# Kernel tuning notes

Measured on AMD Instinct MI355X. Metric: run time of the kernel, lower is better.

The kernel has to match this reference:

```python
import jax, jax.numpy as jnp
import numpy as np

DIM = 256
HEADS = 8
DK = DIM // HEADS
MLP_HID = 4 * DIM
EPS = 1e-5


def _ln(t, s, b):
    m = jnp.mean(t, axis=-1, keepdims=True)
    v = jnp.mean((t - m) ** 2, axis=-1, keepdims=True)
    return (t - m) / jnp.sqrt(v + EPS) * s + b


def setup_inputs() -> dict:
    key = jax.random.key(0)
    ks = jax.random.split(key, 32)
    B, N, C = 8, 128, DIM
    d = {}
    d["x"] = jax.random.normal(ks[0], (B, N, C), jnp.float32)
    d["y"] = jax.random.normal(ks[1], (B, N, N, C), jnp.float32)
    def lin(k, fi, fo):
        k1, k2 = jax.random.split(k)
        return (jax.random.normal(k1, (fi, fo), jnp.float32) * 0.02,
                jax.random.normal(k2, (fo,), jnp.float32) * 0.02)
    for i, nm in enumerate(["q", "k", "v", "e", "oe", "on"]):
        w, b = lin(ks[2 + i], C, C)
        d[f"W{nm}"], d[f"b{nm}"] = w, b
    for i, nm in enumerate(["mlp1", "mlp2"]):
        w1, b1 = lin(ks[10 + 2 * i], C, MLP_HID)
        w2, b2 = lin(ks[11 + 2 * i], MLP_HID, C)
        d[f"{nm}_w1"], d[f"{nm}_b1"] = w1, b1
        d[f"{nm}_w2"], d[f"{nm}_b2"] = w2, b2
    for i, nm in enumerate(["ln1", "ln3", "ln4", "ln5", "ln6"]):
        d[f"{nm}_s"] = jnp.ones((C,), jnp.float32)
        d[f"{nm}_b"] = jnp.zeros((C,), jnp.float32)
    return d


def reference(x, y, Wq, bq, Wk, bk, Wv, bv, We, be, Woe, boe, Won, bon,
              mlp1_w1, mlp1_b1, mlp1_w2, mlp1_b2,
              mlp2_w1, mlp2_b1, mlp2_w2, mlp2_b2,
              ln1_s, ln1_b, ln3_s, ln3_b, ln4_s, ln4_b,
              ln5_s, ln5_b, ln6_s, ln6_b):
    B, N, C = x.shape
    H, DKl = HEADS, DK

    x1 = _ln(x, ln1_s, ln1_b)

    # attention (elementwise q*k modulated by edge embeddings)
    q = (x1 @ Wq + bq).reshape(B, N, H, DKl)
    k = (x1 @ Wk + bk).reshape(B, N, H, DKl)
    v = (x1 @ Wv + bv).reshape(B, N, H, DKl)
    e = (y @ We + be).reshape(B, N, N, H, DKl)

    attn = q[:, :, None] * k[:, None, :]          # (B,N,N,H,DK)
    attn = attn / jnp.sqrt(jnp.float32(DKl))
    attn = attn * (e + 1.0) * e

    edge_out = attn.reshape(B, N, N, C) @ Woe + boe  # out_e
    p = jax.nn.softmax(attn, axis=2)                 # softmax over second n
    agg = jnp.einsum("bijhd,bjhd->bihd", p, v).reshape(B, N, C)
    node_out = agg @ Won + bon                       # out_n

    x2 = _ln(x1 + node_out, ln3_s, ln3_b)
    y2 = _ln(edge_out + y, ln4_s, ln4_b)

    mlp_x = jax.nn.relu(x2 @ mlp1_w1 + mlp1_b1) @ mlp1_w2 + mlp1_b2
    mlp_y = jax.nn.relu(y2 @ mlp2_w1 + mlp2_b1) @ mlp2_w2 + mlp2_b2

    x_out = _ln(x2 + mlp_x, ln5_s, ln5_b)
    y_out = _ln(y2 + mlp_y, ln6_s, ln6_b)
    return (x_out, y_out)
```

## Files before the change

kernel.cpp:

```cpp
#include <hip/hip_runtime.h>

#define CDIM 256
#define NSEQ 128
#define HID 1024
#define EPS 1e-5f
#define SCALE 0.17677669529663687f
#define ASTR 264
#define MROWS 32

typedef __attribute__((ext_vector_type(8))) short short8;
typedef __attribute__((ext_vector_type(4))) float f32x4;

static __device__ __forceinline__ unsigned short f2bf(float x) {
    unsigned u = __float_as_uint(x);
    u += 0x7fff + ((u >> 16) & 1);
    return (unsigned short)(u >> 16);
}
static __device__ __forceinline__ float bf2f(unsigned short h) {
    return __uint_as_float(((unsigned)h) << 16);
}

__global__ __launch_bounds__(256) void prep_all(
    const float* __restrict__ We, const float* __restrict__ Woe,
    const float* __restrict__ W1, const float* __restrict__ W2,
    unsigned short* __restrict__ WeH, unsigned short* __restrict__ WeL,
    unsigned short* __restrict__ WoH, unsigned short* __restrict__ W1H,
    unsigned short* __restrict__ W2H) {
    int blk = blockIdx.x;
    const float* W; unsigned short* H; unsigned short* L = nullptr;
    int N, ksBits, base;
    if (blk < 256)       { W = We;  H = WeH; L = WeL; N = 256;  ksBits = 3; base = 0; }
    else if (blk < 512)  { W = Woe; H = WoH; N = 256;  ksBits = 3; base = 256; }
    else if (blk < 1536) { W = W1;  H = W1H; N = 1024; ksBits = 3; base = 512; }
    else                 { W = W2;  H = W2H; N = 256;  ksBits = 5; base = 1536; }
    int idx = (blk - base) * 256 + threadIdx.x;
    int j = idx & 7, lane = (idx >> 3) & 63, rest = idx >> 9;
    int ks = rest & ((1 << ksBits) - 1), nt = rest >> ksBits;
    int n  = nt * 16 + (lane & 15);
    int kk = ks * 32 + ((lane >> 4) << 3) + j;
    float x = W[kk * N + n];
    unsigned short h = f2bf(x);
    H[idx] = h;
    if (L) L[idx] = f2bf(x - bf2f(h));
}

__global__ __launch_bounds__(256) void lnqkv_kernel(
    const float* __restrict__ x,
    const float* __restrict__ ln1s, const float* __restrict__ ln1b,
    const float* __restrict__ Wq, const float* __restrict__ bq,
    const float* __restrict__ Wk, const float* __restrict__ bk,
    const float* __restrict__ Wv, const float* __restrict__ bv,
    float* __restrict__ x1,
    float* __restrict__ q, float* __restrict__ k, float* __restrict__ v) {
    __shared__ float sX[4][CDIM];
    __shared__ float sMu[4], sRs[4];
    const int bi0 = blockIdx.x * 4, t = threadIdx.x;
    const int w = t >> 6, lane = t & 63;
    float xv[4];
    #pragma unroll
    for (int r = 0; r < 4; ++r) { xv[r] = x[(bi0 + r) * CDIM + t]; sX[r][t] = xv[r]; }
    __syncthreads();
    {
        float s = 0.f, ss = 0.f;
        #pragma unroll
        for (int m = 0; m < 4; ++m) { float a = sX[w][lane + 64 * m]; s += a; ss += a * a; }
        #pragma unroll
        for (int off = 32; off; off >>= 1) { s += __shfl_xor(s, off); ss += __shfl_xor(ss, off); }
        if (lane == 0) {
            float mu = s * (1.f / 256.f);
            sMu[w] = mu;
            sRs[w] = rsqrtf(ss * (1.f / 256.f) - mu * mu + EPS);
        }
    }
    __syncthreads();
    #pragma unroll
    for (int r = 0; r < 4; ++r) {
        float xn = (xv[r] - sMu[r]) * sRs[r] * ln1s[t] + ln1b[t];
        sX[r][t] = xn;
        x1[(bi0 + r) * CDIM + t] = xn;
    }
    __syncthreads();
    float aq[4], ak[4], av[4];
    #pragma unroll
    for (int r = 0; r < 4; ++r) { aq[r] = bq[t]; ak[r] = bk[t]; av[r] = bv[t]; }
    #pragma unroll 4
    for (int kk = 0; kk < CDIM; ++kk) {
        float wq = Wq[kk * CDIM + t], wk = Wk[kk * CDIM + t], wv = Wv[kk * CDIM + t];
        #pragma unroll
        for (int r = 0; r < 4; ++r) {
            float xd = sX[r][kk];
            aq[r] += xd * wq; ak[r] += xd * wk; av[r] += xd * wv;
        }
    }
    #pragma unroll
    for (int r = 0; r < 4; ++r) {
        q[(bi0 + r) * CDIM + t] = aq[r];
        k[(bi0 + r) * CDIM + t] = ak[r];
        v[(bi0 + r) * CDIM + t] = av[r];
    }
}

template <int TERMS>
static __device__ __forceinline__ void gemmN(
    const unsigned short* Ah, const unsigned short* Al,
    const unsigned short* __restrict__ Bh, const unsigned short* __restrict__ Bl,
    int nt0, int ksTotal, int ks0, int lane, f32x4 acc[2][2])
{
    const int l16 = lane & 15, quad = lane >> 4;
    #pragma unroll 2
    for (int ks = 0; ks < 8; ++ks) {
        short8 bh[2], bl[2];
        #pragma unroll
        for (int nt = 0; nt < 2; ++nt) {
            size_t off = ((size_t)((nt0 + nt) * ksTotal + (ks0 + ks)) * 64 + lane) * 8;
            bh[nt] = *(const short8*)(Bh + off);
            if (TERMS == 3) bl[nt] = *(const short8*)(Bl + off);
        }
        #pragma unroll
        for (int mt = 0; mt < 2; ++mt) {
            int ao = (mt * 16 + l16) * ASTR + ks * 32 + quad * 8;
            short8 ah = *(const short8*)(Ah + ao);
            short8 al = *(const short8*)(Al + ao);
            #pragma unroll
            for (int nt = 0; nt < 2; ++nt) {
                acc[mt][nt] = __builtin_amdgcn_mfma_f32_16x16x32_bf16(ah, bh[nt], acc[mt][nt], 0, 0, 0);
                acc[mt][nt] = __builtin_amdgcn_mfma_f32_16x16x32_bf16(al, bh[nt], acc[mt][nt], 0, 0, 0);
                if (TERMS == 3)
                    acc[mt][nt] = __builtin_amdgcn_mfma_f32_16x16x32_bf16(ah, bl[nt], acc[mt][nt], 0, 0, 0);
            }
        }
    }
}

static __device__ __forceinline__ void ln_reduce32(
    float pre[2][2][4], float* sSum, float* sSS, int w, int l16, int quad, int tid)
{
    #pragma unroll
    for (int mt = 0; mt < 2; ++mt)
        #pragma unroll
        for (int r = 0; r < 4; ++r) {
            float s  = pre[mt][0][r] + pre[mt][1][r];
            float ss = pre[mt][0][r] * pre[mt][0][r] + pre[mt][1][r] * pre[mt][1][r];
            #pragma unroll
            for (int off = 1; off < 16; off <<= 1) {
                s  += __shfl_xor(s, off);
                ss += __shfl_xor(ss, off);
            }
            if (l16 == 0) {
                int row = mt * 16 + quad * 4 + r;
                sSum[w * 32 + row] = s;
                sSS [w * 32 + row] = ss;
            }
        }
    __syncthreads();
    if (tid < 32) {
        float S = 0.f, SS2 = 0.f;
        #pragma unroll
        for (int ww = 0; ww < 8; ++ww) { S += sSum[ww * 32 + tid]; SS2 += sSS[ww * 32 + tid]; }
        float mu = S * (1.f / 256.f);
        float rs = rsqrtf(SS2 * (1.f / 256.f) - mu * mu + EPS);
        sSum[tid] = mu; sSS[tid] = rs;
    }
    __syncthreads();
}

__global__ __launch_bounds__(512, 4) void y_mega(
    const float* __restrict__ y, const float* __restrict__ qg, const float* __restrict__ kg,
    const unsigned short* __restrict__ WeH, const unsigned short* __restrict__ WeL,
    const float* __restrict__ be,
    const unsigned short* __restrict__ WoH, const float* __restrict__ boe,
    const unsigned short* __restrict__ W1H, const float* __restrict__ b1,
    const unsigned short* __restrict__ W2H, const float* __restrict__ b2,
    const float* __restrict__ ln4s, const float* __restrict__ ln4b,
    const float* __restrict__ ln6s, const float* __restrict__ ln6b,
    unsigned short* __restrict__ attn_bf, float* __restrict__ yout)
{
    __shared__ unsigned short sAh[MROWS * ASTR], sAl[MROWS * ASTR];
    __shared__ unsigned short sHh[MROWS * ASTR], sHl[MROWS * ASTR];
    __shared__ float sSum[8 * 32], sSS[8 * 32];

    const int tid  = threadIdx.x;
    const int w    = tid >> 6, lane = tid & 63;
    const int l16  = lane & 15, quad = lane >> 4;
    const long long row0 = (long long)blockIdx.x * MROWS;
    const int b  = (int)(row0 >> 14);
    const int i  = (int)((row0 >> 7) & 127);
    const int j0 = (int)(row0 & 127);
    const float* qrow  = qg + ((b << 7) + i) * CDIM;
    const float* kbase = kg + ((b << 7) + j0) * CDIM;
    const int c0 = w * 32 + l16, c1 = c0 + 16;

    {
        int r  = tid >> 4;
        int cc = (tid & 15) * 16;
        const float* src = y + (row0 + r) * CDIM + cc;
        unsigned short hbuf[16], lbuf[16];
        #pragma unroll
        for (int e = 0; e < 16; e += 4) {
            float4 vv = *(const float4*)(src + e);
            float a[4] = {vv.x, vv.y, vv.z, vv.w};
            #pragma unroll
            for (int d = 0; d < 4; ++d) {
                unsigned short h = f2bf(a[d]);
                hbuf[e + d] = h;
                lbuf[e + d] = f2bf(a[d] - bf2f(h));
            }
        }
        #pragma unroll
        for (int e = 0; e < 16; e += 8) {
            *(short8*)&sAh[r * ASTR + cc + e] = *(short8*)&hbuf[e];
            *(short8*)&sAl[r * ASTR + cc + e] = *(short8*)&lbuf[e];
        }
    }
    __syncthreads();

    f32x4 acc[2][2];
    const f32x4 zf = {0.f, 0.f, 0.f, 0.f};

    #pragma unroll
    for (int mt = 0; mt < 2; ++mt) { acc[mt][0] = zf; acc[mt][1] = zf; }
    gemmN<3>(sAh, sAl, WeH, WeL, w * 2, 8, 0, lane, acc);

    float q0 = qrow[c0], q1 = qrow[c1];
    float be0 = be[c0], be1 = be[c1];
    float attnv[2][2][4];
    #pragma unroll
    for (int mt = 0; mt < 2; ++mt)
        #pragma unroll
        for (int r = 0; r < 4; ++r) {
            int mloc = mt * 16 + quad * 4 + r;
            float k0 = kbase[mloc * CDIM + c0], k1 = kbase[mloc * CDIM + c1];
            float e0 = acc[mt][0][r] + be0, e1 = acc[mt][1][r] + be1;
            float a0 = q0 * k0 * SCALE * ((e0 + 1.f) * e0);
            float a1 = q1 * k1 * SCALE * ((e1 + 1.f) * e1);
            attnv[mt][0][r] = a0; attnv[mt][1][r] = a1;
            attn_bf[(row0 + mloc) * CDIM + c0] = f2bf(a0);
            attn_bf[(row0 + mloc) * CDIM + c1] = f2bf(a1);
        }
    __syncthreads();

    #pragma unroll
    for (int mt = 0; mt < 2; ++mt)
        #pragma unroll
        for (int r = 0; r < 4; ++r) {
            int mloc = mt * 16 + quad * 4 + r;
            #pragma unroll
            for (int nt = 0; nt < 2; ++nt) {
                int c = (nt == 0) ? c0 : c1;
                float a = attnv[mt][nt][r];
                unsigned short h = f2bf(a);
                sAh[mloc * ASTR + c] = h;
                sAl[mloc * ASTR + c] = f2bf(a - bf2f(h));
            }
        }
    __syncthreads();

    #pragma unroll
    for (int mt = 0; mt < 2; ++mt) { acc[mt][0] = zf; acc[mt][1] = zf; }
    gemmN<2>(sAh, sAl, WoH, nullptr, w * 2, 8, 0, lane, acc);

    float pre[2][2][4];
    float bo0 = boe[c0], bo1 = boe[c1];
    #pragma unroll
    for (int mt = 0; mt < 2; ++mt)
        #pragma unroll
        for (int r = 0; r < 4; ++r) {
            int mloc = mt * 16 + quad * 4 + r;
            pre[mt][0][r] = acc[mt][0][r] + bo0 + y[(row0 + mloc) * CDIM + c0];
            pre[mt][1][r] = acc[mt][1][r] + bo1 + y[(row0 + mloc) * CDIM + c1];
        }
    ln_reduce32(pre, sSum, sSS, w, l16, quad, tid);

    float l4s0 = ln4s[c0], l4b0 = ln4b[c0], l4s1 = ln4s[c1], l4b1 = ln4b[c1];
    float y2v[2][2][4];
    #pragma unroll
    for (int mt = 0; mt < 2; ++mt)
        #pragma unroll
        for (int r = 0; r < 4; ++r) {
            int mloc = mt * 16 + quad * 4 + r;
            float mu = sSum[mloc], rs = sSS[mloc];
            float v0 = (pre[mt][0][r] - mu) * rs * l4s0 + l4b0;
            float v1 = (pre[mt][1][r] - mu) * rs * l4s1 + l4b1;
            y2v[mt][0][r] = v0; y2v[mt][1][r] = v1;
            unsigned short h0 = f2bf(v0), h1 = f2bf(v1);
            sAh[mloc * ASTR + c0] = h0; sAl[mloc * ASTR + c0] = f2bf(v0 - bf2f(h0));
            sAh[mloc * ASTR + c1] = h1; sAl[mloc * ASTR + c1] = f2bf(v1 - bf2f(h1));
        }
    __syncthreads();

    f32x4 out[2][2];
    #pragma unroll
    for (int mt = 0; mt < 2; ++mt) { out[mt][0] = zf; out[mt][1] = zf; }
    for (int qq = 0; qq < 4; ++qq) {
        f32x4 hh[2][2];
        #pragma unroll
        for (int mt = 0; mt < 2; ++mt) { hh[mt][0] = zf; hh[mt][1] = zf; }
        gemmN<2>(sAh, sAl, W1H, nullptr, qq * 16 + w * 2, 8, 0, lane, hh);
        float bb0 = b1[qq * 256 + c0], bb1 = b1[qq * 256 + c1];
        __syncthreads();
        #pragma unroll
        for (int mt = 0; mt < 2; ++mt)
            #pragma unroll
            for (int r = 0; r < 4; ++r) {
                int mloc = mt * 16 + quad * 4 + r;
                float h0 = fmaxf(hh[mt][0][r] + bb0, 0.f);
                float h1 = fmaxf(hh[mt][1][r] + bb1, 0.f);
                unsigned short hb0 = f2bf(h0), hb1 = f2bf(h1);
                sHh[mloc * ASTR + c0] = hb0; sHl[mloc * ASTR + c0] = f2bf(h0 - bf2f(hb0));
                sHh[mloc * ASTR + c1] = hb1; sHl[mloc * ASTR + c1] = f2bf(h1 - bf2f(hb1));
            }
        __syncthreads();
        gemmN<2>(sHh, sHl, W2H, nullptr, w * 2, 32, qq * 8, lane, out);
    }

    float b20 = b2[c0], b21 = b2[c1];
    #pragma unroll
    for (int mt = 0; mt < 2; ++mt)
        #pragma unroll
        for (int r = 0; r < 4; ++r) {
            pre[mt][0][r] = y2v[mt][0][r] + out[mt][0][r] + b20;
            pre[mt][1][r] = y2v[mt][1][r] + out[mt][1][r] + b21;
        }
    ln_reduce32(pre, sSum, sSS, w, l16, quad, tid);

    float l6s0 = ln6s[c0], l6b0 = ln6b[c0], l6s1 = ln6s[c1], l6b1 = ln6b[c1];
    #pragma unroll
    for (int mt = 0; mt < 2; ++mt)
        #pragma unroll
        for (int r = 0; r < 4; ++r) {
            int mloc = mt * 16 + quad * 4 + r;
            float mu = sSum[mloc], rs = sSS[mloc];
            yout[(row0 + mloc) * CDIM + c0] = (pre[mt][0][r] - mu) * rs * l6s0 + l6b0;
            yout[(row0 + mloc) * CDIM + c1] = (pre[mt][1][r] - mu) * rs * l6s1 + l6b1;
        }
}

__global__ __launch_bounds__(256) void softmax_agg(
    const unsigned short* __restrict__ attn, const float* __restrict__ v,
    float* __restrict__ agg) {
    __shared__ float2 sM[2][128], sS[2][128], sO[2][128];
    const int bi = blockIdx.x, t = threadIdx.x;
    const int c2 = t & 127, team = t >> 7, ch = c2 * 2;
    const unsigned short* ap = attn + (size_t)bi * NSEQ * CDIM + ch;
    const float* vp = v + (size_t)(bi >> 7) * NSEQ * CDIM + ch;
    const int jb = team * 64;
    float m0 = -1e30f, m1 = -1e30f;
    #pragma unroll 4
    for (int j = jb; j < jb + 64; ++j) {
        unsigned uu = *(const unsigned*)(ap + (size_t)j * CDIM);
        m0 = fmaxf(m0, bf2f((unsigned short)uu));
        m1 = fmaxf(m1, bf2f((unsigned short)(uu >> 16)));
    }
    sM[team][c2] = make_float2(m0, m1);
    __syncthreads();
    float2 mo = sM[team ^ 1][c2];
    m0 = fmaxf(m0, mo.x); m1 = fmaxf(m1, mo.y);
    float s0 = 0.f, s1 = 0.f, o0 = 0.f, o1 = 0.f;
    #pragma unroll 4
    for (int j = jb; j < jb + 64; ++j) {
        unsigned uu = *(const unsigned*)(ap + (size_t)j * CDIM);
        float e0 = __expf(bf2f((unsigned short)uu) - m0);
        float e1 = __expf(bf2f((unsigned short)(uu >> 16)) - m1);
        float2 vv = *(const float2*)(vp + (size_t)j * CDIM);
        s0 += e0; s1 += e1;
        o0 += e0 * vv.x; o1 += e1 * vv.y;
    }
    sS[team][c2] = make_float2(s0, s1);
    sO[team][c2] = make_float2(o0, o1);
    __syncthreads();
    if (team == 0) {
        float2 s2 = sS[1][c2], o2 = sO[1][c2];
        float r0 = (o0 + o2.x) / (s0 + s2.x);
        float r1 = (o1 + o2.y) / (s1 + s2.y);
        *(float2*)(agg + (size_t)bi * CDIM + ch) = make_float2(r0, r1);
    }
}

__global__ __launch_bounds__(256) void x_path(
    const float* __restrict__ x1, const float* __restrict__ agg,
    const float* __restrict__ Won, const float* __restrict__ bon,
    const float* __restrict__ ln3s, const float* __restrict__ ln3b,
    const float* __restrict__ w1, const float* __restrict__ b1,
    const float* __restrict__ w2, const float* __restrict__ b2,
    const float* __restrict__ ln5s, const float* __restrict__ ln5b,
    float* __restrict__ xout) {
    __shared__ float sG[4][CDIM];
    __shared__ float sP[4][CDIM];
    __shared__ float sH[4][HID];
    __shared__ float sMu[4], sRs[4];
    const int bi0 = blockIdx.x * 4, t = threadIdx.x;
    const int w = t >> 6, lane = t & 63;
    #pragma unroll
    for (int r = 0; r < 4; ++r) sG[r][t] = agg[(bi0 + r) * CDIM + t];
    __syncthreads();
    float no[4];
    #pragma unroll
    for (int r = 0; r < 4; ++r) no[r] = bon[t];
    #pragma unroll 4
    for (int kk = 0; kk < CDIM; ++kk) {
        float wv = Won[kk * CDIM + t];
        #pragma unroll
        for (int r = 0; r < 4; ++r) no[r] += sG[r][kk] * wv;
    }
    float pre[4];
    #pragma unroll
    for (int r = 0; r < 4; ++r) {
        pre[r] = x1[(bi0 + r) * CDIM + t] + no[r];
        sP[r][t] = pre[r];
    }
    __syncthreads();
    {
        float s = 0.f, ss = 0.f;
        #pragma unroll
        for (int m = 0; m < 4; ++m) { float a = sP[w][lane + 64 * m]; s += a; ss += a * a; }
        #pragma unroll
        for (int off = 32; off; off >>= 1) { s += __shfl_xor(s, off); ss += __shfl_xor(ss, off); }
        if (lane == 0) {
            float mu = s * (1.f / 256.f);
            sMu[w] = mu; sRs[w] = rsqrtf(ss * (1.f / 256.f) - mu * mu + EPS);
        }
    }
    __syncthreads();
    float x2[4];
    #pragma unroll
    for (int r = 0; r < 4; ++r) {
        x2[r] = (pre[r] - sMu[r]) * sRs[r] * ln3s[t] + ln3b[t];
        sP[r][t] = x2[r];
    }
    __syncthreads();
    float h[4][4];
    #pragma unroll
    for (int m = 0; m < 4; ++m) {
        float bb = b1[t + 256 * m];
        #pragma unroll
        for (int r = 0; r < 4; ++r) h[r][m] = bb;
    }
    #pragma unroll 2
    for (int kk = 0; kk < CDIM; ++kk) {
        float wv[4];
        #pragma unroll
        for (int m = 0; m < 4; ++m) wv[m] = w1[kk * HID + t + 256 * m];
        #pragma unroll
        for (int r = 0; r < 4; ++r) {
            float xd = sP[r][kk];
            #pragma unroll
            for (int m = 0; m < 4; ++m) h[r][m] += xd * wv[m];
        }
    }
    #pragma unroll
    for (int r = 0; r < 4; ++r)
        #pragma unroll
        for (int m = 0; m < 4; ++m) sH[r][t + 256 * m] = fmaxf(h[r][m], 0.f);
    __syncthreads();
    float o[4];
    #pragma unroll
    for (int r = 0; r < 4; ++r) o[r] = b2[t];
    #pragma unroll 4
    for (int u = 0; u < HID; ++u) {
        float wv = w2[u * CDIM + t];
        #pragma unroll
        for (int r = 0; r < 4; ++r) o[r] += sH[r][u] * wv;
    }
    float pre2[4];
    #pragma unroll
    for (int r = 0; r < 4; ++r) { pre2[r] = x2[r] + o[r]; sP[r][t] = pre2[r]; }
    __syncthreads();
    {
        float s = 0.f, ss = 0.f;
        #pragma unroll
        for (int m = 0; m < 4; ++m) { float a = sP[w][lane + 64 * m]; s += a; ss += a * a; }
        #pragma unroll
        for (int off = 32; off; off >>= 1) { s += __shfl_xor(s, off); ss += __shfl_xor(ss, off); }
        if (lane == 0) {
            float mu = s * (1.f / 256.f);
            sMu[w] = mu; sRs[w] = rsqrtf(ss * (1.f / 256.f) - mu * mu + EPS);
        }
    }
    __syncthreads();
    #pragma unroll
    for (int r = 0; r < 4; ++r)
        xout[(bi0 + r) * CDIM + t] = (pre2[r] - sMu[r]) * sRs[r] * ln5s[t] + ln5b[t];
}

extern "C" void kernel_launch(void* const* d_in, const int* in_sizes, int n_in,
                              void* d_out, int out_size, void* d_ws, size_t ws_size,
                              hipStream_t stream) {
    const float* x   = (const float*)d_in[0];
    const float* y   = (const float*)d_in[1];
    const float* Wq  = (const float*)d_in[2];  const float* bq  = (const float*)d_in[3];
    const float* Wk  = (const float*)d_in[4];  const float* bk  = (const float*)d_in[5];
    const float* Wv  = (const float*)d_in[6];  const float* bv  = (const float*)d_in[7];
    const float* We  = (const float*)d_in[8];  const float* be  = (const float*)d_in[9];
    const float* Woe = (const float*)d_in[10]; const float* boe = (const float*)d_in[11];
    const float* Won = (const float*)d_in[12]; const float* bon = (const float*)d_in[13];
    const float* m1w1= (const float*)d_in[14]; const float* m1b1= (const float*)d_in[15];
    const float* m1w2= (const float*)d_in[16]; const float* m1b2= (const float*)d_in[17];
    const float* m2w1= (const float*)d_in[18]; const float* m2b1= (const float*)d_in[19];
    const float* m2w2= (const float*)d_in[20]; const float* m2b2= (const float*)d_in[21];
    const float* ln1s= (const float*)d_in[22]; const float* ln1b= (const float*)d_in[23];
    const float* ln3s= (const float*)d_in[24]; const float* ln3b= (const float*)d_in[25];
    const float* ln4s= (const float*)d_in[26]; const float* ln4b= (const float*)d_in[27];
    const float* ln5s= (const float*)d_in[28]; const float* ln5b= (const float*)d_in[29];
    const float* ln6s= (const float*)d_in[30]; const float* ln6b= (const float*)d_in[31];

    const int BN  = 8 * 128;
    const long long BNN = 8LL * 128 * 128;

    float* ws  = (float*)d_ws;
    float* x1  = ws;
    float* q   = x1 + BN * CDIM;
    float* k   = q  + BN * CDIM;
    float* v   = k  + BN * CDIM;
    float* agg = v  + BN * CDIM;
    unsigned short* attn_bf = (unsigned short*)(agg + BN * CDIM);
    unsigned short* WeH = attn_bf + BNN * CDIM;
    unsigned short* WeL = WeH + 65536;
    unsigned short* WoH = WeL + 65536;
    unsigned short* W1H = WoH + 65536;
    unsigned short* W2H = W1H + 262144;

    float* xout = (float*)d_out;
    float* yout = xout + BN * CDIM;

    prep_all<<<2560, 256, 0, stream>>>(We, Woe, m2w1, m2w2, WeH, WeL, WoH, W1H, W2H);
    lnqkv_kernel<<<BN / 4, 256, 0, stream>>>(x, ln1s, ln1b, Wq, bq, Wk, bk, Wv, bv,
                                             x1, q, k, v);
    y_mega<<<(int)(BNN / MROWS), 512, 0, stream>>>(
        y, q, k, WeH, WeL, be, WoH, boe, W1H, m2b1, W2H, m2b2,
        ln4s, ln4b, ln6s, ln6b, attn_bf, yout);
    softmax_agg<<<BN, 256, 0, stream>>>(attn_bf, v, agg);
    x_path<<<BN / 4, 256, 0, stream>>>(x1, agg, Won, bon, ln3s, ln3b,
                                       m1w1, m1b1, m1w2, m1b2, ln5s, ln5b, xout);
}
```

Before: 880.3 us.

## Restructure y_mega to 4 waves with 64-column tiles and XOR-swizzled LDS

The fused edge kernel goes from 8 waves owning 32 columns each to 4 waves owning 64 columns each, so every A-fragment read from LDS feeds twice as many MFMAs. Padded LDS rows are replaced by an XOR swizzle, and the MLP hidden chunk shrinks to 128 columns, which cuts shared memory. bf16 hi/lo splits now use the packed v_cvt_pk_bf16_f32 instruction. In exchange each thread holds more accumulators, which raises register pressure, and fewer waves per block may hide latency less well.

```diff
diff --git a/kernel.cpp b/kernel.cpp
--- a/kernel.cpp
+++ b/kernel.cpp
@@ -5,7 +5,6 @@
 #define HID 1024
 #define EPS 1e-5f
 #define SCALE 0.17677669529663687f
-#define ASTR 264
 #define MROWS 32
 
 typedef __attribute__((ext_vector_type(8))) short short8;
@@ -19,6 +18,14 @@
 static __device__ __forceinline__ float bf2f(unsigned short h) {
     return __uint_as_float(((unsigned)h) << 16);
 }
+
+static __device__ __forceinline__ unsigned cvt_pk(float a, float b) {
+    unsigned r;
+    asm("v_cvt_pk_bf16_f32 %0, %1, %2" : "=v"(r) : "v"(a), "v"(b));
+    return r;
+}
+
+static __device__ __forceinline__ int swz(int row) { return (row ^ (row >> 2)) & 7; }
 
 __global__ __launch_bounds__(256) void prep_all(
     const float* __restrict__ We, const float* __restrict__ Woe,
@@ -100,29 +107,30 @@
     }
 }
 
-template <int TERMS>
+template <int TERMS, int NT, int KS, int LDA>
 static __device__ __forceinline__ void gemmN(
     const unsigned short* Ah, const unsigned short* Al,
     const unsigned short* __restrict__ Bh, const unsigned short* __restrict__ Bl,
-    int nt0, int ksTotal, int ks0, int lane, f32x4 acc[2][2])
+    int nt0, int ksTotal, int ks0, int lane, f32x4 acc[2][NT])
 {
     const int l16 = lane & 15, quad = lane >> 4;
     #pragma unroll 2
-    for (int ks = 0; ks < 8; ++ks) {
-        short8 bh[2], bl[2];
-        #pragma unroll
-        for (int nt = 0; nt < 2; ++nt) {
+    for (int ks = 0; ks < KS; ++ks) {
+        short8 bh[NT], bl[NT];
+        #pragma unroll
+        for (int nt = 0; nt < NT; ++nt) {
             size_t off = ((size_t)((nt0 + nt) * ksTotal + (ks0 + ks)) * 64 + lane) * 8;
             bh[nt] = *(const short8*)(Bh + off);
             if (TERMS == 3) bl[nt] = *(const short8*)(Bl + off);
         }
         #pragma unroll
         for (int mt = 0; mt < 2; ++mt) {
-            int ao = (mt * 16 + l16) * ASTR + ks * 32 + quad * 8;
+            const int row = mt * 16 + l16;
+            const int ao  = row * LDA + (((ks * 4 + quad) ^ swz(row)) << 3);
             short8 ah = *(const short8*)(Ah + ao);
             short8 al = *(const short8*)(Al + ao);
             #pragma unroll
-            for (int nt = 0; nt < 2; ++nt) {
+            for (int nt = 0; nt < NT; ++nt) {
                 acc[mt][nt] = __builtin_amdgcn_mfma_f32_16x16x32_bf16(ah, bh[nt], acc[mt][nt], 0, 0, 0);
                 acc[mt][nt] = __builtin_amdgcn_mfma_f32_16x16x32_bf16(al, bh[nt], acc[mt][nt], 0, 0, 0);
                 if (TERMS == 3)
@@ -132,15 +140,19 @@
     }
 }
 
-static __device__ __forceinline__ void ln_reduce32(
-    float pre[2][2][4], float* sSum, float* sSS, int w, int l16, int quad, int tid)
+static __device__ __forceinline__ void ln_reduce32_4w(
+    float pre[2][4][4], float* sSum, float* sSS, int w, int l16, int quad, int tid)
 {
     #pragma unroll
     for (int mt = 0; mt < 2; ++mt)
         #pragma unroll
         for (int r = 0; r < 4; ++r) {
-            float s  = pre[mt][0][r] + pre[mt][1][r];
-            float ss = pre[mt][0][r] * pre[mt][0][r] + pre[mt][1][r] * pre[mt][1][r];
+            float s = 0.f, ss = 0.f;
+            #pragma unroll
+            for (int nt = 0; nt < 4; ++nt) {
+                float a = pre[mt][nt][r];
+                s += a; ss += a * a;
+            }
             #pragma unroll
             for (int off = 1; off < 16; off <<= 1) {
                 s  += __shfl_xor(s, off);
@@ -156,7 +168,7 @@
     if (tid < 32) {
         float S = 0.f, SS2 = 0.f;
         #pragma unroll
-        for (int ww = 0; ww < 8; ++ww) { S += sSum[ww * 32 + tid]; SS2 += sSS[ww * 32 + tid]; }
+        for (int ww = 0; ww < 4; ++ww) { S += sSum[ww * 32 + tid]; SS2 += sSS[ww * 32 + tid]; }
         float mu = S * (1.f / 256.f);
         float rs = rsqrtf(SS2 * (1.f / 256.f) - mu * mu + EPS);
         sSum[tid] = mu; sSS[tid] = rs;
@@ -164,7 +176,7 @@
     __syncthreads();
 }
 
-__global__ __launch_bounds__(512, 4) void y_mega(
+__global__ __launch_bounds__(256, 3) void y_mega(
     const float* __restrict__ y, const float* __restrict__ qg, const float* __restrict__ kg,
     const unsigned short* __restrict__ WeH, const unsigned short* __restrict__ WeL,
     const float* __restrict__ be,
@@ -175,9 +187,9 @@
     const float* __restrict__ ln6s, const float* __restrict__ ln6b,
     unsigned short* __restrict__ attn_bf, float* __restrict__ yout)
 {
-    __shared__ unsigned short sAh[MROWS * ASTR], sAl[MROWS * ASTR];
-    __shared__ unsigned short sHh[MROWS * ASTR], sHl[MROWS * ASTR];
-    __shared__ float sSum[8 * 32], sSS[8 * 32];
+    __shared__ __align__(16) unsigned short sAh[32 * 256], sAl[32 * 256];
+    __shared__ __align__(16) unsigned short sHh[32 * 128], sHl[32 * 128];
+    __shared__ float sSum[4 * 32], sSS[4 * 32];
 
     const int tid  = threadIdx.x;
     const int w    = tid >> 6, lane = tid & 63;
@@ -188,150 +200,196 @@
     const int j0 = (int)(row0 & 127);
     const float* qrow  = qg + ((b << 7) + i) * CDIM;
     const float* kbase = kg + ((b << 7) + j0) * CDIM;
-    const int c0 = w * 32 + l16, c1 = c0 + 16;
+    int c[4];
+    #pragma unroll
+    for (int nt = 0; nt < 4; ++nt) c[nt] = w * 64 + nt * 16 + l16;
 
     {
-        int r  = tid >> 4;
-        int cc = (tid & 15) * 16;
-        const float* src = y + (row0 + r) * CDIM + cc;
-        unsigned short hbuf[16], lbuf[16];
-        #pragma unroll
-        for (int e = 0; e < 16; e += 4) {
-            float4 vv = *(const float4*)(src + e);
-            float a[4] = {vv.x, vv.y, vv.z, vv.w};
-            #pragma unroll
-            for (int d = 0; d < 4; ++d) {
-                unsigned short h = f2bf(a[d]);
-                hbuf[e + d] = h;
-                lbuf[e + d] = f2bf(a[d] - bf2f(h));
-            }
-        }
-        #pragma unroll
-        for (int e = 0; e < 16; e += 8) {
-            *(short8*)&sAh[r * ASTR + cc + e] = *(short8*)&hbuf[e];
-            *(short8*)&sAl[r * ASTR + cc + e] = *(short8*)&lbuf[e];
-        }
-    }
-    __syncthreads();
-
-    f32x4 acc[2][2];
+        const int r  = tid >> 3;
+        const int cb = (tid & 7) * 32;
+        const int fr = swz(r);
+        const float* src = y + (row0 + r) * CDIM + cb;
+        #pragma unroll
+        for (int gi = 0; gi < 4; ++gi) {
+            float4 v0 = *(const float4*)(src + gi * 8);
+            float4 v1 = *(const float4*)(src + gi * 8 + 4);
+            float a[8] = {v0.x, v0.y, v0.z, v0.w, v1.x, v1.y, v1.z, v1.w};
+            unsigned hw[4], lw[4];
+            #pragma unroll
+            for (int p = 0; p < 4; ++p) {
+                unsigned ph = cvt_pk(a[2 * p], a[2 * p + 1]);
+                float r0 = a[2 * p]     - __uint_as_float(ph << 16);
+                float r1 = a[2 * p + 1] - __uint_as_float(ph & 0xffff0000u);
+                hw[p] = ph;
+                lw[p] = cvt_pk(r0, r1);
+            }
+            const int gs = ((cb >> 3) + gi) ^ fr;
+            *(uint4*)&sAh[r * 256 + gs * 8] = *(const uint4*)hw;
+            *(uint4*)&sAl[r * 256 + gs * 8] = *(const uint4*)lw;
+        }
+    }
+    __syncthreads();
+
     const f32x4 zf = {0.f, 0.f, 0.f, 0.f};
-
-    #pragma unroll
-    for (int mt = 0; mt < 2; ++mt) { acc[mt][0] = zf; acc[mt][1] = zf; }
-    gemmN<3>(sAh, sAl, WeH, WeL, w * 2, 8, 0, lane, acc);
-
-    float q0 = qrow[c0], q1 = qrow[c1];
-    float be0 = be[c0], be1 = be[c1];
-    float attnv[2][2][4];
-    #pragma unroll
-    for (int mt = 0; mt < 2; ++mt)
-        #pragma unroll
-        for (int r = 0; r < 4; ++r) {
-            int mloc = mt * 16 + quad * 4 + r;
-            float k0 = kbase[mloc * CDIM + c0], k1 = kbase[mloc * CDIM + c1];
-            float e0 = acc[mt][0][r] + be0, e1 = acc[mt][1][r] + be1;
-            float a0 = q0 * k0 * SCALE * ((e0 + 1.f) * e0);
-            float a1 = q1 * k1 * SCALE * ((e1 + 1.f) * e1);
-            attnv[mt][0][r] = a0; attnv[mt][1][r] = a1;
-            attn_bf[(row0 + mloc) * CDIM + c0] = f2bf(a0);
-            attn_bf[(row0 + mloc) * CDIM + c1] = f2bf(a1);
-        }
-    __syncthreads();
-
-    #pragma unroll
-    for (int mt = 0; mt < 2; ++mt)
-        #pragma unroll
-        for (int r = 0; r < 4; ++r) {
-            int mloc = mt * 16 + quad * 4 + r;
-            #pragma unroll
-            for (int nt = 0; nt < 2; ++nt) {
-                int c = (nt == 0) ? c0 : c1;
-                float a = attnv[mt][nt][r];
-                unsigned short h = f2bf(a);
-                sAh[mloc * ASTR + c] = h;
-                sAl[mloc * ASTR + c] = f2bf(a - bf2f(h));
-            }
-        }
-    __syncthreads();
-
-    #pragma unroll
-    for (int mt = 0; mt < 2; ++mt) { acc[mt][0] = zf; acc[mt][1] = zf; }
-    gemmN<2>(sAh, sAl, WoH, nullptr, w * 2, 8, 0, lane, acc);
-
-    float pre[2][2][4];
-    float bo0 = boe[c0], bo1 = boe[c1];
-    #pragma unroll
-    for (int mt = 0; mt < 2; ++mt)
-        #pragma unroll
-        for (int r = 0; r < 4; ++r) {
-            int mloc = mt * 16 + quad * 4 + r;
-            pre[mt][0][r] = acc[mt][0][r] + bo0 + y[(row0 + mloc) * CDIM + c0];
-            pre[mt][1][r] = acc[mt][1][r] + bo1 + y[(row0 + mloc) * CDIM + c1];
-        }
-    ln_reduce32(pre, sSum, sSS, w, l16, quad, tid);
-
-    float l4s0 = ln4s[c0], l4b0 = ln4b[c0], l4s1 = ln4s[c1], l4b1 = ln4b[c1];
-    float y2v[2][2][4];
-    #pragma unroll
-    for (int mt = 0; mt < 2; ++mt)
-        #pragma unroll
-        for (int r = 0; r < 4; ++r) {
-            int mloc = mt * 16 + quad * 4 + r;
-            float mu = sSum[mloc], rs = sSS[mloc];
-            float v0 = (pre[mt][0][r] - mu) * rs * l4s0 + l4b0;
-            float v1 = (pre[mt][1][r] - mu) * rs * l4s1 + l4b1;
-            y2v[mt][0][r] = v0; y2v[mt][1][r] = v1;
-            unsigned short h0 = f2bf(v0), h1 = f2bf(v1);
-            sAh[mloc * ASTR + c0] = h0; sAl[mloc * ASTR + c0] = f2bf(v0 - bf2f(h0));
-            sAh[mloc * ASTR + c1] = h1; sAl[mloc * ASTR + c1] = f2bf(v1 - bf2f(h1));
-        }
-    __syncthreads();
-
-    f32x4 out[2][2];
-    #pragma unroll
-    for (int mt = 0; mt < 2; ++mt) { out[mt][0] = zf; out[mt][1] = zf; }
-    for (int qq = 0; qq < 4; ++qq) {
+    f32x4 acc[2][4];
+
+    #pragma unroll
+    for (int mt = 0; mt < 2; ++mt)
+        #pragma unroll
+        for (int nt = 0; nt < 4; ++nt) acc[mt][nt] = zf;
+    gemmN<3, 4, 8, 256>(sAh, sAl, WeH, WeL, w * 4, 8, 0, lane, acc);
+
+    float qv[4], bev[4];
+    #pragma unroll
+    for (int nt = 0; nt < 4; ++nt) { qv[nt] = qrow[c[nt]]; bev[nt] = be[c[nt]]; }
+    float attnv[2][4][4];
+    #pragma unroll
+    for (int mt = 0; mt < 2; ++mt)
+        #pragma unroll
+        for (int r = 0; r < 4; ++r) {
+            const int mloc = mt * 16 + quad * 4 + r;
+            const float* krow = kbase + mloc * CDIM;
+            #pragma unroll
+            for (int nt = 0; nt < 4; ++nt) {
+                float e = acc[mt][nt][r] + bev[nt];
+                attnv[mt][nt][r] = qv[nt] * krow[c[nt]] * SCALE * ((e + 1.f) * e);
+            }
+        }
+    __syncthreads();
+
+    #pragma unroll
+    for (int mt = 0; mt < 2; ++mt)
+        #pragma unroll
+        for (int r = 0; r < 4; ++r) {
+            const int mloc = mt * 16 + quad * 4 + r;
+            const int fr2  = swz(mloc);
+            unsigned short* gout = attn_bf + (row0 + mloc) * CDIM;
+            #pragma unroll
+            for (int np = 0; np < 4; np += 2) {
+                float a0 = attnv[mt][np][r], a1 = attnv[mt][np + 1][r];
+                unsigned ph = cvt_pk(a0, a1);
+                float r0 = a0 - __uint_as_float(ph << 16);
+                float r1 = a1 - __uint_as_float(ph & 0xffff0000u);
+                unsigned pl = cvt_pk(r0, r1);
+                const int aA = mloc * 256 + (((c[np]     >> 3) ^ fr2) << 3) + (l16 & 7);
+                const int aB = mloc * 256 + (((c[np + 1] >> 3) ^ fr2) << 3) + (l16 & 7);
+                sAh[aA] = (unsigned short)ph;  sAh[aB] = (unsigned short)(ph >> 16);
+                sAl[aA] = (unsigned short)pl;  sAl[aB] = (unsigned short)(pl >> 16);
+                gout[c[np]]     = (unsigned short)ph;
+                gout[c[np + 1]] = (unsigned short)(ph >> 16);
+            }
+        }
+    __syncthreads();
+
+    #pragma unroll
+    for (int mt = 0; mt < 2; ++mt)
+        #pragma unroll
+        for (int nt = 0; nt < 4; ++nt) acc[mt][nt] = zf;
+    gemmN<2, 4, 8, 256>(sAh, sAl, WoH, nullptr, w * 4, 8, 0, lane, acc);
+
+    float pre[2][4][4];
+    float bov[4];
+    #pragma unroll
+    for (int nt = 0; nt < 4; ++nt) bov[nt] = boe[c[nt]];
+    #pragma unroll
+    for (int mt = 0; mt < 2; ++mt)
+        #pragma unroll
+        for (int r = 0; r < 4; ++r) {
+            const int mloc = mt * 16 + quad * 4 + r;
+            const float* yrow = y + (row0 + mloc) * CDIM;
+            #pragma unroll
+            for (int nt = 0; nt < 4; ++nt)
+                pre[mt][nt][r] = acc[mt][nt][r] + bov[nt] + yrow[c[nt]];
+        }
+    ln_reduce32_4w(pre, sSum, sSS, w, l16, quad, tid);
+
+    float l4sv[4], l4bv[4];
+    #pragma unroll
+    for (int nt = 0; nt < 4; ++nt) { l4sv[nt] = ln4s[c[nt]]; l4bv[nt] = ln4b[c[nt]]; }
+    float y2v[2][4][4];
+    #pragma unroll
+    for (int mt = 0; mt < 2; ++mt)
+        #pragma unroll
+        for (int r = 0; r < 4; ++r) {
+            const int mloc = mt * 16 + quad * 4 + r;
+            const int fr2  = swz(mloc);
+            const float mu = sSum[mloc], rs = sSS[mloc];
+            #pragma unroll
+            for (int np = 0; np < 4; np += 2) {
+                float v0 = (pre[mt][np][r]     - mu) * rs * l4sv[np]     + l4bv[np];
+                float v1 = (pre[mt][np + 1][r] - mu) * rs * l4sv[np + 1] + l4bv[np + 1];
+                y2v[mt][np][r] = v0; y2v[mt][np + 1][r] = v1;
+                unsigned ph = cvt_pk(v0, v1);
+                float r0 = v0 - __uint_as_float(ph << 16);
+                float r1 = v1 - __uint_as_float(ph & 0xffff0000u);
+                unsigned pl = cvt_pk(r0, r1);
+                const int aA = mloc * 256 + (((c[np]     >> 3) ^ fr2) << 3) + (l16 & 7);
+                const int aB = mloc * 256 + (((c[np + 1] >> 3) ^ fr2) << 3) + (l16 & 7);
+                sAh[aA] = (unsigned short)ph;  sAh[aB] = (unsigned short)(ph >> 16);
+                sAl[aA] = (unsigned short)pl;  sAl[aB] = (unsigned short)(pl >> 16);
+            }
+        }
+    __syncthreads();
+
+    f32x4 out[2][4];
+    #pragma unroll
+    for (int mt = 0; mt < 2; ++mt)
+        #pragma unroll
+        for (int nt = 0; nt < 4; ++nt) out[mt][nt] = zf;
+    const int hc0 = w * 32 + l16, hc1 = hc0 + 16;
+    for (int ch = 0; ch < 8; ++ch) {
         f32x4 hh[2][2];
         #pragma unroll
         for (int mt = 0; mt < 2; ++mt) { hh[mt][0] = zf; hh[mt][1] = zf; }
-        gemmN<2>(sAh, sAl, W1H, nullptr, qq * 16 + w * 2, 8, 0, lane, hh);
-        float bb0 = b1[qq * 256 + c0], bb1 = b1[qq * 256 + c1];
+        gemmN<2, 2, 8, 256>(sAh, sAl, W1H, nullptr, ch * 8 + w * 2, 8, 0, lane, hh);
+        float bb0 = b1[ch * 128 + hc0], bb1 = b1[ch * 128 + hc1];
         __syncthreads();
         #pragma unroll
         for (int mt = 0; mt < 2; ++mt)
             #pragma unroll
             for (int r = 0; r < 4; ++r) {
-                int mloc = mt * 16 + quad * 4 + r;
+                const int mloc = mt * 16 + quad * 4 + r;
+                const int fr2  = swz(mloc);
                 float h0 = fmaxf(hh[mt][0][r] + bb0, 0.f);
                 float h1 = fmaxf(hh[mt][1][r] + bb1, 0.f);
-                unsigned short hb0 = f2bf(h0), hb1 = f2bf(h1);
-                sHh[mloc * ASTR + c0] = hb0; sHl[mloc * ASTR + c0] = f2bf(h0 - bf2f(hb0));
-                sHh[mloc * ASTR + c1] = hb1; sHl[mloc * ASTR + c1] = f2bf(h1 - bf2f(hb1));
+                unsigned ph = cvt_pk(h0, h1);
+                float r0 = h0 - __uint_as_float(ph << 16);
+                float r1 = h1 - __uint_as_float(ph & 0xffff0000u);
+                unsigned pl = cvt_pk(r0, r1);
+                const int aA = mloc * 128 + (((hc0 >> 3) ^ fr2) << 3) + (hc0 & 7);
+                const int aB = mloc * 128 + (((hc1 >> 3) ^ fr2) << 3) + (hc1 & 7);
+                sHh[aA] = (unsigned short)ph;  sHh[aB] = (unsigned short)(ph >> 16);
+                sHl[aA] = (unsigned short)pl;  sHl[aB] = (unsigned short)(pl >> 16);
             }
         __syncthreads();
-        gemmN<2>(sHh, sHl, W2H, nullptr, w * 2, 32, qq * 8, lane, out);
-    }
-
-    float b20 = b2[c0], b21 = b2[c1];
-    #pragma unroll
-    for (int mt = 0; mt < 2; ++mt)
-        #pragma unroll
-        for (int r = 0; r < 4; ++r) {
-            pre[mt][0][r] = y2v[mt][0][r] + out[mt][0][r] + b20;
-            pre[mt][1][r] = y2v[mt][1][r] + out[mt][1][r] + b21;
-        }
-    ln_reduce32(pre, sSum, sSS, w, l16, quad, tid);
-
-    float l6s0 = ln6s[c0], l6b0 = ln6b[c0], l6s1 = ln6s[c1], l6b1 = ln6b[c1];
-    #pragma unroll
-    for (int mt = 0; mt < 2; ++mt)
-        #pragma unroll
-        for (int r = 0; r < 4; ++r) {
-            int mloc = mt * 16 + quad * 4 + r;
-            float mu = sSum[mloc], rs = sSS[mloc];
-            yout[(row0 + mloc) * CDIM + c0] = (pre[mt][0][r] - mu) * rs * l6s0 + l6b0;
-            yout[(row0 + mloc) * CDIM + c1] = (pre[mt][1][r] - mu) * rs * l6s1 + l6b1;
+        gemmN<2, 4, 4, 128>(sHh, sHl, W2H, nullptr, w * 4, 32, ch * 4, lane, out);
+    }
+
+    float b2v[4];
+    #pragma unroll
+    for (int nt = 0; nt < 4; ++nt) b2v[nt] = b2[c[nt]];
+    #pragma unroll
+    for (int mt = 0; mt < 2; ++mt)
+        #pragma unroll
+        for (int r = 0; r < 4; ++r)
+            #pragma unroll
+            for (int nt = 0; nt < 4; ++nt)
+                pre[mt][nt][r] = y2v[mt][nt][r] + out[mt][nt][r] + b2v[nt];
+    ln_reduce32_4w(pre, sSum, sSS, w, l16, quad, tid);
+
+    float l6sv[4], l6bv[4];
+    #pragma unroll
+    for (int nt = 0; nt < 4; ++nt) { l6sv[nt] = ln6s[c[nt]]; l6bv[nt] = ln6b[c[nt]]; }
+    #pragma unroll
+    for (int mt = 0; mt < 2; ++mt)
+        #pragma unroll
+        for (int r = 0; r < 4; ++r) {
+            const int mloc = mt * 16 + quad * 4 + r;
+            const float mu = sSum[mloc], rs = sSS[mloc];
+            float* orow = yout + (row0 + mloc) * CDIM;
+            #pragma unroll
+            for (int nt = 0; nt < 4; ++nt)
+                orow[c[nt]] = (pre[mt][nt][r] - mu) * rs * l6sv[nt] + l6bv[nt];
         }
 }
 
@@ -525,7 +583,7 @@
     prep_all<<<2560, 256, 0, stream>>>(We, Woe, m2w1, m2w2, WeH, WeL, WoH, W1H, W2H);
     lnqkv_kernel<<<BN / 4, 256, 0, stream>>>(x, ln1s, ln1b, Wq, bq, Wk, bk, Wv, bv,
                                              x1, q, k, v);
-    y_mega<<<(int)(BNN / MROWS), 512, 0, stream>>>(
+    y_mega<<<(int)(BNN / MROWS), 256, 0, stream>>>(
         y, q, k, WeH, WeL, be, WoH, boe, W1H, m2b1, W2H, m2b2,
         ln4s, ln4b, ln6s, ln6b, attn_bf, yout);
     softmax_agg<<<BN, 256, 0, stream>>>(attn_bf, v, agg);
```

After: 971.0 us. 1.1x slower.

## Swizzle LDS operand tiles and pack bf16 hi/lo splits with paired lanes

Applied to the files above, without the earlier changes.

Replaces the padded shared-memory stride with an unpadded 256-wide layout and an XOR swizzle on 8-element groups. This is meant to avoid bank conflicts on the MFMA A-operand reads. The bf16 hi/lo split now uses the packed v_cvt_pk_bf16_f32 instruction, and neighbouring lanes exchange values by shuffle. Even lanes write the packed high plane and odd lanes the packed low plane, each as one 32-bit store, which cuts the number of conversions and scalar 16-bit stores. The cost is more shuffle traffic and an inline asm dependency on this instruction being available on the target.

```diff
diff --git a/kernel.cpp b/kernel.cpp
--- a/kernel.cpp
+++ b/kernel.cpp
@@ -5,7 +5,6 @@
 #define HID 1024
 #define EPS 1e-5f
 #define SCALE 0.17677669529663687f
-#define ASTR 264
 #define MROWS 32
 
 typedef __attribute__((ext_vector_type(8))) short short8;
@@ -19,6 +18,15 @@
 static __device__ __forceinline__ float bf2f(unsigned short h) {
     return __uint_as_float(((unsigned)h) << 16);
 }
+static __device__ __forceinline__ unsigned cvt_pk(float a, float b) {
+    unsigned r;
+    asm("v_cvt_pk_bf16_f32 %0, %1, %2" : "=v"(r) : "v"(a), "v"(b));
+    return r;
+}
+static __device__ __forceinline__ float lo16f(unsigned u) { return __uint_as_float(u << 16); }
+static __device__ __forceinline__ float hi16f(unsigned u) { return __uint_as_float(u & 0xffff0000u); }
+
+static __device__ __forceinline__ int swz(int row) { return (row ^ (row >> 2)) & 7; }
 
 __global__ __launch_bounds__(256) void prep_all(
     const float* __restrict__ We, const float* __restrict__ Woe,
@@ -118,7 +126,8 @@
         }
         #pragma unroll
         for (int mt = 0; mt < 2; ++mt) {
-            int ao = (mt * 16 + l16) * ASTR + ks * 32 + quad * 8;
+            const int row = mt * 16 + l16;
+            const int ao  = row * 256 + (((ks * 4 + quad) ^ swz(row)) << 3);
             short8 ah = *(const short8*)(Ah + ao);
             short8 al = *(const short8*)(Al + ao);
             #pragma unroll
@@ -164,6 +173,27 @@
     __syncthreads();
 }
 
+static __device__ __forceinline__ unsigned pair_pack(float v, bool odd, unsigned* ph_out) {
+    float part = __shfl_xor(v, 1);
+    float lo = odd ? part : v;
+    float hi = odd ? v : part;
+    unsigned ph = cvt_pk(lo, hi);
+    *ph_out = ph;
+    if (odd) {
+        float rlo = lo - lo16f(ph);
+        float rhi = hi - hi16f(ph);
+        return cvt_pk(rlo, rhi);
+    }
+    return ph;
+}
+static __device__ __forceinline__ void plane_store(
+    unsigned short* Hp, unsigned short* Lp, int row, int c, unsigned pk, bool odd) {
+    const int p = c & ~1;
+    const int idx = row * 256 + ((((p >> 3) ^ swz(row)) << 3)) + (p & 7);
+    if (!odd) *(unsigned*)&Hp[idx] = pk;
+    else      *(unsigned*)&Lp[idx] = pk;
+}
+
 __global__ __launch_bounds__(512, 4) void y_mega(
     const float* __restrict__ y, const float* __restrict__ qg, const float* __restrict__ kg,
     const unsigned short* __restrict__ WeH, const unsigned short* __restrict__ WeL,
@@ -175,13 +205,14 @@
     const float* __restrict__ ln6s, const float* __restrict__ ln6b,
     unsigned short* __restrict__ attn_bf, float* __restrict__ yout)
 {
-    __shared__ unsigned short sAh[MROWS * ASTR], sAl[MROWS * ASTR];
-    __shared__ unsigned short sHh[MROWS * ASTR], sHl[MROWS * ASTR];
+    __shared__ __align__(16) unsigned short sAh[32 * 256], sAl[32 * 256];
+    __shared__ __align__(16) unsigned short sHh[32 * 256], sHl[32 * 256];
     __shared__ float sSum[8 * 32], sSS[8 * 32];
 
     const int tid  = threadIdx.x;
     const int w    = tid >> 6, lane = tid & 63;
     const int l16  = lane & 15, quad = lane >> 4;
+    const bool odd = (l16 & 1) != 0;
     const long long row0 = (long long)blockIdx.x * MROWS;
     const int b  = (int)(row0 >> 14);
     const int i  = (int)((row0 >> 7) & 127);
@@ -191,25 +222,27 @@
     const int c0 = w * 32 + l16, c1 = c0 + 16;
 
     {
-        int r  = tid >> 4;
-        int cc = (tid & 15) * 16;
+        const int r  = tid >> 4;
+        const int cc = (tid & 15) * 16;
+        const int fr = swz(r);
         const float* src = y + (row0 + r) * CDIM + cc;
-        unsigned short hbuf[16], lbuf[16];
-        #pragma unroll
-        for (int e = 0; e < 16; e += 4) {
-            float4 vv = *(const float4*)(src + e);
-            float a[4] = {vv.x, vv.y, vv.z, vv.w};
-            #pragma unroll
-            for (int d = 0; d < 4; ++d) {
-                unsigned short h = f2bf(a[d]);
-                hbuf[e + d] = h;
-                lbuf[e + d] = f2bf(a[d] - bf2f(h));
-            }
-        }
         #pragma unroll
         for (int e = 0; e < 16; e += 8) {
-            *(short8*)&sAh[r * ASTR + cc + e] = *(short8*)&hbuf[e];
-            *(short8*)&sAl[r * ASTR + cc + e] = *(short8*)&lbuf[e];
+            float4 v0 = *(const float4*)(src + e);
+            float4 v1 = *(const float4*)(src + e + 4);
+            unsigned h0 = cvt_pk(v0.x, v0.y);
+            unsigned h1 = cvt_pk(v0.z, v0.w);
+            unsigned h2 = cvt_pk(v1.x, v1.y);
+            unsigned h3 = cvt_pk(v1.z, v1.w);
+            unsigned L0 = cvt_pk(v0.x - lo16f(h0), v0.y - hi16f(h0));
+            unsigned L1 = cvt_pk(v0.z - lo16f(h1), v0.w - hi16f(h1));
+            unsigned L2 = cvt_pk(v1.x - lo16f(h2), v1.y - hi16f(h2));
+            unsigned L3 = cvt_pk(v1.z - lo16f(h3), v1.w - hi16f(h3));
+            const int gs = (((cc + e) >> 3) ^ fr);
+            uint4 hv; hv.x = h0; hv.y = h1; hv.z = h2; hv.w = h3;
+            uint4 lv; lv.x = L0; lv.y = L1; lv.z = L2; lv.w = L3;
+            *(uint4*)&sAh[r * 256 + gs * 8] = hv;
+            *(uint4*)&sAl[r * 256 + gs * 8] = lv;
         }
     }
     __syncthreads();
@@ -223,35 +256,33 @@
 
     float q0 = qrow[c0], q1 = qrow[c1];
     float be0 = be[c0], be1 = be[c1];
-    float attnv[2][2][4];
-    #pragma unroll
-    for (int mt = 0; mt < 2; ++mt)
-        #pragma unroll
-        for (int r = 0; r < 4; ++r) {
-            int mloc = mt * 16 + quad * 4 + r;
-            float k0 = kbase[mloc * CDIM + c0], k1 = kbase[mloc * CDIM + c1];
-            float e0 = acc[mt][0][r] + be0, e1 = acc[mt][1][r] + be1;
-            float a0 = q0 * k0 * SCALE * ((e0 + 1.f) * e0);
-            float a1 = q1 * k1 * SCALE * ((e1 + 1.f) * e1);
-            attnv[mt][0][r] = a0; attnv[mt][1][r] = a1;
-            attn_bf[(row0 + mloc) * CDIM + c0] = f2bf(a0);
-            attn_bf[(row0 + mloc) * CDIM + c1] = f2bf(a1);
-        }
-    __syncthreads();
-
-    #pragma unroll
-    for (int mt = 0; mt < 2; ++mt)
-        #pragma unroll
-        for (int r = 0; r < 4; ++r) {
-            int mloc = mt * 16 + quad * 4 + r;
+    unsigned pk1[2][2][4];
+    #pragma unroll
+    for (int mt = 0; mt < 2; ++mt)
+        #pragma unroll
+        for (int r = 0; r < 4; ++r) {
+            const int mloc = mt * 16 + quad * 4 + r;
+            const float* krow = kbase + mloc * CDIM;
+            unsigned short* gout = attn_bf + (row0 + mloc) * CDIM;
             #pragma unroll
             for (int nt = 0; nt < 2; ++nt) {
-                int c = (nt == 0) ? c0 : c1;
-                float a = attnv[mt][nt][r];
-                unsigned short h = f2bf(a);
-                sAh[mloc * ASTR + c] = h;
-                sAl[mloc * ASTR + c] = f2bf(a - bf2f(h));
+                const int c = (nt == 0) ? c0 : c1;
+                float e = acc[mt][nt][r] + ((nt == 0) ? be0 : be1);
+                float a = ((nt == 0) ? q0 : q1) * krow[c] * SCALE * ((e + 1.f) * e);
+                unsigned ph;
+                pk1[mt][nt][r] = pair_pack(a, odd, &ph);
+                if (!odd) *(unsigned*)&gout[c & ~1] = ph;
             }
+        }
+    __syncthreads();
+
+    #pragma unroll
+    for (int mt = 0; mt < 2; ++mt)
+        #pragma unroll
+        for (int r = 0; r < 4; ++r) {
+            const int mloc = mt * 16 + quad * 4 + r;
+            plane_store(sAh, sAl, mloc, c0, pk1[mt][0][r], odd);
+            plane_store(sAh, sAl, mloc, c1, pk1[mt][1][r], odd);
         }
     __syncthreads();
 
@@ -265,7 +296,7 @@
     for (int mt = 0; mt < 2; ++mt)
         #pragma unroll
         for (int r = 0; r < 4; ++r) {
-            int mloc = mt * 16 + quad * 4 + r;
+            const int mloc = mt * 16 + quad * 4 + r;
             pre[mt][0][r] = acc[mt][0][r] + bo0 + y[(row0 + mloc) * CDIM + c0];
             pre[mt][1][r] = acc[mt][1][r] + bo1 + y[(row0 + mloc) * CDIM + c1];
         }
@@ -277,14 +308,16 @@
     for (int mt = 0; mt < 2; ++mt)
         #pragma unroll
         for (int r = 0; r < 4; ++r) {
-            int mloc = mt * 16 + quad * 4 + r;
-            float mu = sSum[mloc], rs = sSS[mloc];
+            const int mloc = mt * 16 + quad * 4 + r;
+            const float mu = sSum[mloc], rs = sSS[mloc];
             float v0 = (pre[mt][0][r] - mu) * rs * l4s0 + l4b0;
             float v1 = (pre[mt][1][r] - mu) * rs * l4s1 + l4b1;
             y2v[mt][0][r] = v0; y2v[mt][1][r] = v1;
-            unsigned short h0 = f2bf(v0), h1 = f2bf(v1);
-            sAh[mloc * ASTR + c0] = h0; sAl[mloc * ASTR + c0] = f2bf(v0 - bf2f(h0));
-            sAh[mloc * ASTR + c1] = h1; sAl[mloc * ASTR + c1] = f2bf(v1 - bf2f(h1));
+            unsigned ph;
+            unsigned p0 = pair_pack(v0, odd, &ph);
+            unsigned p1 = pair_pack(v1, odd, &ph);
+            plane_store(sAh, sAl, mloc, c0, p0, odd);
+            plane_store(sAh, sAl, mloc, c1, p1, odd);
         }
     __syncthreads();
 
@@ -302,12 +335,14 @@
         for (int mt = 0; mt < 2; ++mt)
             #pragma unroll
             for (int r = 0; r < 4; ++r) {
-                int mloc = mt * 16 + quad * 4 + r;
+                const int mloc = mt * 16 + quad * 4 + r;
                 float h0 = fmaxf(hh[mt][0][r] + bb0, 0.f);
                 float h1 = fmaxf(hh[mt][1][r] + bb1, 0.f);
-                unsigned short hb0 = f2bf(h0), hb1 = f2bf(h1);
-                sHh[mloc * ASTR + c0] = hb0; sHl[mloc * ASTR + c0] = f2bf(h0 - bf2f(hb0));
-                sHh[mloc * ASTR + c1] = hb1; sHl[mloc * ASTR + c1] = f2bf(h1 - bf2f(hb1));
+                unsigned ph;
+                unsigned p0 = pair_pack(h0, odd, &ph);
+                unsigned p1 = pair_pack(h1, odd, &ph);
+                plane_store(sHh, sHl, mloc, c0, p0, odd);
+                plane_store(sHh, sHl, mloc, c1, p1, odd);
             }
         __syncthreads();
         gemmN<2>(sHh, sHl, W2H, nullptr, w * 2, 32, qq * 8, lane, out);
@@ -328,8 +363,8 @@
     for (int mt = 0; mt < 2; ++mt)
         #pragma unroll
         for (int r = 0; r < 4; ++r) {
-            int mloc = mt * 16 + quad * 4 + r;
-            float mu = sSum[mloc], rs = sSS[mloc];
+            const int mloc = mt * 16 + quad * 4 + r;
+            const float mu = sSum[mloc], rs = sSS[mloc];
             yout[(row0 + mloc) * CDIM + c0] = (pre[mt][0][r] - mu) * rs * l6s0 + l6b0;
             yout[(row0 + mloc) * CDIM + c1] = (pre[mt][1][r] - mu) * rs * l6s1 + l6b1;
         }
```

Measured after the change: 953.0 us. 8.3% more time.
